# Kernel optimization log

Measured on AMD Instinct MI355X. Metric: run time of the kernel, lower is better.

Reference implementation:

```python
import jax, jax.numpy as jnp
import numpy as np
from jax import lax

B, N, FIN, T, K, FC, FT = 8, 2048, 3, 12, 3, 64, 64


def _conv2d(x, w, b, pad):
    # x [B,C,N,T], w [O,I,1,kw], NCHW conv
    y = lax.conv_general_dilated(x, w, (1, 1), pad,
                                 dimension_numbers=('NCHW', 'OIHW', 'NCHW'))
    return y + b[None, :, None, None]


def _spatial_att(h, W, a, alpha, concat):
    # GAT-style dense attention. h [B,N,Fin], W [Fin,D], a [2D,1]
    D = W.shape[1]
    Wh = h @ W                                             # [B,N,D]
    e = jax.nn.leaky_relu(Wh @ a[:D] + jnp.swapaxes(Wh @ a[D:], 1, 2), alpha)  # [B,N,N]
    att = jax.nn.softmax(jax.nn.sigmoid(e), axis=1)        # softmax over dim=1 (as in torch)
    hp = jnp.einsum('bij,bjd->bid', att, Wh)
    return jax.nn.elu(hp) if concat else hp


def setup_inputs() -> dict:
    key = jax.random.key(0)
    ks = jax.random.split(key, 24)
    rnd = lambda i, shape, scale=1.0: (jax.random.normal(ks[i], shape, dtype=jnp.float32) * scale)
    FTm = FC * T  # 768 spatial-attention feature dim
    D = FTm // 2
    return {
        'x': rnd(0, (B, N, FIN, T)),
        'cheb': rnd(1, (K, N, N), 1.0 / np.sqrt(N)),
        'Gamma': rnd(2, (K, FIN, FC), 1.0 / np.sqrt(FIN)),
        'W_heads': rnd(3, (2, FTm, D), 1.0 / np.sqrt(FTm)),
        'a_heads': rnd(4, (2, 2 * D, 1), 1.0 / np.sqrt(2 * D)),
        'W_out': rnd(5, (FTm, FTm), 1.0 / np.sqrt(FTm)),
        'a_out': rnd(6, (2 * FTm, 1), 1.0 / np.sqrt(2 * FTm)),
        'U1': rnd(7, (FT, FT), 1.0 / np.sqrt(FT)),
        'U2': rnd(8, (FT,), 1.0 / np.sqrt(FT)),
        'U3': rnd(9, (FT,), 1.0 / np.sqrt(FT)),
        'be': rnd(10, (1, T, T), 0.1),
        'Ve': rnd(11, (T, T), 1.0 / np.sqrt(T)),
        'time_w': rnd(12, (FT, FC, 1, 3), 1.0 / np.sqrt(3 * FC)),
        'time_b': rnd(13, (FT,), 0.01),
        'res_w': rnd(14, (FT, FIN, 1, 1), 1.0 / np.sqrt(FIN)),
        'res_b': rnd(15, (FT,), 0.01),
        'back_w': rnd(16, (FT, FC, 1, 3), 1.0 / np.sqrt(3 * FC)),
        'back_b': rnd(17, (FT,), 0.01),
        'fore_w': rnd(18, (FT, FC, 1, 3), 1.0 / np.sqrt(3 * FC)),
        'fore_b': rnd(19, (FT,), 0.01),
        'ln_g': jnp.ones((FT,), jnp.float32),
        'ln_b': jnp.zeros((FT,), jnp.float32),
    }


def reference(x, cheb, Gamma, W_heads, a_heads, W_out, a_out, U1, U2, U3, be, Ve,
              time_w, time_b, res_w, res_b, back_w, back_b, fore_w, fore_b, ln_g, ln_b):
    b, n, fin, t = x.shape
    k_ = cheb.shape[0]
    fc = Gamma.shape[2]
    # ChebNetII interpolation coefficients T_k(x_j), x_j = cos((j+0.5)pi/K) -> [j,k]
    jj = np.arange(k_)
    cxj = jnp.asarray(np.cos(np.outer((jj + 0.5) * np.pi / k_, np.arange(k_))), x.dtype)
    lhs = jnp.einsum('jio,jk->kio', Gamma, cxj)                         # [K,Fin,Fc]
    rhs = jnp.einsum('bnit,knm->kbmit', x, cheb)                        # [K,B,N,Fin,T]
    spatial_gcn = jax.nn.relu((2.0 / (k_ + 1)) * jnp.einsum('kbmit,kio->bmot', rhs, lhs))  # [B,N,Fc,T]

    # Spatial transformer: 2 GAT heads + output attention
    h = spatial_gcn.reshape(b, n, fc * t)
    heads = jax.vmap(lambda W, a: _spatial_att(h, W, a, 0.1, True))(W_heads, a_heads)  # [H,B,N,D]
    hcat = jnp.transpose(heads, (1, 2, 0, 3)).reshape(b, n, -1)
    gcn_SAt = jax.nn.relu(_spatial_att(hcat, W_out, a_out, 0.1, False)).reshape(b, n, fc, t)

    # Temporal conv (1x3, pad 1)
    tc = _conv2d(jnp.transpose(gcn_SAt, (0, 2, 1, 3)), time_w, time_b, ((0, 0), (1, 1)))
    tc = jnp.transpose(tc, (0, 2, 1, 3))                                # [B,N,Ft,T]

    # Temporal attention
    lhs_t = jnp.einsum('bnft,fg,g->btn', tc, U1, U2)                    # [B,T,N]
    rhs_t = jnp.einsum('f,bnft->bnt', U3, tc)                           # [B,N,T]
    prod = jnp.einsum('bsn,bnt->bst', lhs_t, rhs_t)                     # [B,T,T]
    E = jnp.einsum('is,bst->bit', Ve, jax.nn.sigmoid(prod + be))
    E = jax.nn.softmax(E, axis=1)
    tcn = jnp.einsum('bnft,bts->bnfs', tc, E)                           # [B,N,Ft,T]

    # Residual (1x1 conv) + LayerNorm over channel dim
    x_res = _conv2d(jnp.transpose(x, (0, 2, 1, 3)), res_w, res_b, ((0, 0), (0, 0)))
    x_res = jnp.transpose(x_res, (0, 2, 1, 3))                          # [B,N,Ft,T]
    z = jnp.transpose(jax.nn.relu(x_res + tcn), (0, 3, 1, 2))           # [B,T,N,Ft]
    mu = z.mean(-1, keepdims=True)
    var = z.var(-1, keepdims=True)
    z = (z - mu) / jnp.sqrt(var + 1e-5) * ln_g + ln_b
    result = jnp.transpose(z, (0, 2, 3, 1))                             # [B,N,Ft,T]

    rp = jnp.transpose(result, (0, 2, 1, 3))
    backcast = jnp.transpose(_conv2d(rp, back_w, back_b, ((0, 0), (1, 1))), (0, 2, 1, 3))
    forecast = jnp.transpose(_conv2d(rp, fore_w, fore_b, ((0, 0), (1, 1))), (0, 2, 1, 3))
    return (backcast, forecast)
```

## Files before the change

kernel.cpp:

```cpp
#include <hip/hip_runtime.h>


typedef unsigned short u16;
typedef __bf16 bf16x8 __attribute__((ext_vector_type(8)));
typedef float f32x4 __attribute__((ext_vector_type(4)));
typedef u16 u16x8 __attribute__((ext_vector_type(8)));

__device__ __forceinline__ u16 f2b(float f) {
  union { float f; unsigned u; } v; v.f = f;
  unsigned u = v.u;
  u = u + 0x7FFFu + ((u >> 16) & 1u);
  return (u16)(u >> 16);
}
__device__ __forceinline__ float b2f(u16 h) {
  union { unsigned u; float f; } v; v.u = ((unsigned)h) << 16; return v.f;
}
__device__ __forceinline__ float qfun(float x) {
  float e = x > 0.f ? x : 0.1f * x;
  float s = __builtin_amdgcn_rcpf(1.f + __expf(-e));
  return __expf(s);
}

template <int N> __device__ __forceinline__ void waitvm() {
  if constexpr (N == 0)      asm volatile("s_waitcnt vmcnt(0)" ::: "memory");
  else if constexpr (N == 2) asm volatile("s_waitcnt vmcnt(2)" ::: "memory");
  else if constexpr (N == 4) asm volatile("s_waitcnt vmcnt(4)" ::: "memory");
  else if constexpr (N == 6) asm volatile("s_waitcnt vmcnt(6)" ::: "memory");
  else                       asm volatile("s_waitcnt vmcnt(8)" ::: "memory");
}
__device__ __forceinline__ void rawbar() { asm volatile("s_barrier" ::: "memory"); }

#define GLOAD16(g, l) __builtin_amdgcn_global_load_lds( \
    (__attribute__((address_space(1))) void*)(g),       \
    (__attribute__((address_space(3))) void*)(l), 16, 0, 0)

constexpr size_t OFF_LHS     = 0x0;
constexpr size_t OFF_U1U2    = 0x1000;
constexpr size_t OFF_BIASBIG = 0x1100;
constexpr size_t OFF_FH      = 0x3000;
constexpr size_t OFF_GH      = 0x23000;
constexpr size_t OFF_RDH     = 0x43000;
constexpr size_t OFF_FO      = 0x63000;
constexpr size_t OFF_GO      = 0x73000;
constexpr size_t OFF_RDO     = 0x83000;
constexpr size_t OFF_LHST    = 0x93000;
constexpr size_t OFF_RHST    = 0x153000;
constexpr size_t OFF_PROD    = 0x213000;
constexpr size_t OFF_E       = 0x215000;
constexpr size_t OFF_WCATT   = 0x220000;
constexpr size_t OFF_WOUTT   = 0x340000;
constexpr size_t OFF_WTBIG   = 0x460000;
constexpr size_t OFF_XCOLT   = 0x580000;
constexpr size_t OFF_CHEBT   = 0x700000;
constexpr size_t OFF_C1      = 0x1F00000;
constexpr size_t OFF_H       = 0x4300000;
constexpr size_t OFF_P       = 0x700000;
constexpr size_t OFF_WHCATT  = 0x5B00000;
constexpr size_t OFF_HCAT    = 0x7300000;
constexpr size_t OFF_WHOUTT  = 0x5B00000;
constexpr size_t OFF_GCNB    = 0x7300000;
constexpr size_t OFF_WBFBIG  = 0x8B00000;
constexpr size_t OFF_TCS     = 0x700000;
constexpr size_t OFF_RESULTB = 0x3700000;
constexpr size_t WS_NEEDED   = 0x8D40000;

struct GemmP {
  const u16* A; const u16* BT;
  long sA, sB;
  int K, lda, ldb;
  int swz, splitK;
  float* Cf; long sCf; int ldcf;
  u16* Cb;  long sCb; int ldcb;
  u16* CbT; int ldcT; long sCbT;
  const float* bias;
  float* outB; float* outF;
};

template <int EPI, int WN, int AF = 0>
__global__ __launch_bounds__(256, (WN == 1 ? 3 : 2)) void gemm_bf16(GemmP p) {
  constexpr int BUFU  = AF ? (WN == 1 ? 4096 : 8192) : (WN == 1 ? 8192 : 12288);
  constexpr int SMEMU = 3 * BUFU;
  constexpr int LPWB  = AF ? (WN == 1 ? 2 : 4) : (WN == 1 ? 4 : 6);
  constexpr int WVN   = AF ? (LPWB + 4) : LPWB;
  __shared__ u16 smem[SMEMU];
  const int tid  = threadIdx.x;
  const int lane = tid & 63;
  const int wid  = tid >> 6;
  const int wm = wid >> 1, wn = wid & 1;

  long m0, n0;
  int z = blockIdx.z;
  if (p.swz == 2) {
    int nT = gridDim.x;
    int nwg = nT * gridDim.y;
    long L = (long)blockIdx.z * nwg + blockIdx.x + (long)nT * blockIdx.y;
    z = (int)(L & 7);
    long r = L >> 3;
    m0 = (r / nT) * 128;
    n0 = (r % nT) * (128 * WN);
  } else if (p.swz) {
    int nT = gridDim.x;
    int nwg = nT * gridDim.y;
    int lin = blockIdx.x + nT * blockIdx.y;
    int q = nwg >> 3;
    int swz = (lin & 7) * q + (lin >> 3);
    m0 = (long)(swz / nT) * 128;
    n0 = (long)(swz % nT) * (128 * WN);
  } else {
    m0 = (long)blockIdx.y * 128;
    n0 = (long)blockIdx.x * (128 * WN);
  }

  const int K = p.K;
  long aBase, bBase;
  if (p.splitK) {
    int kz = z >> 2, ch = z & 3;
    aBase = (long)kz * p.sA + (long)ch * 512;
    bBase = (long)ch * 512;
  } else {
    aBase = (long)z * p.sA;
    bBase = (long)z * p.sB;
  }
  const u16* Ab = p.A + aBase + m0 * p.lda;
  const u16* Bb = p.BT + bBase + n0 * p.ldb;

  const int sk = (((lane & 3) ^ ((lane >> 3) & 3))) * 8;
  const u16* aP0 = Ab + (long)(wid * 32 + (lane >> 2)) * p.lda + sk;
  const u16* aP1 = aP0 + (long)16 * p.lda;
  const u16* bP0 = Bb + (long)(wid * 32 * WN + (lane >> 2)) * p.ldb + sk;
  const u16* bP1 = bP0 + (long)16 * p.ldb;
  const u16* bP2 = bP0 + (long)32 * p.ldb;
  const u16* bP3 = bP0 + (long)48 * p.ldb;
  const int aslot = wid * 1024;
  const int bslot = (AF ? 0 : 4096) + wid * (WN == 1 ? 1024 : 2048);

  auto STAGE = [&](int s, int bi) {
    long ko = (long)s * 32;
    u16* base = smem + bi * BUFU;
    if constexpr (!AF) {
      GLOAD16(aP0 + ko, base + aslot);
      GLOAD16(aP1 + ko, base + aslot + 512);
    }
    GLOAD16(bP0 + ko, base + bslot);
    GLOAD16(bP1 + ko, base + bslot + 512);
    if constexpr (WN == 2) {
      GLOAD16(bP2 + ko, base + bslot + 1024);
      GLOAD16(bP3 + ko, base + bslot + 1536);
    }
  };

  f32x4 acc[4][4 * WN];
  f32x4 zero = {0.f, 0.f, 0.f, 0.f};
#pragma unroll
  for (int i = 0; i < 4; ++i)
#pragma unroll
    for (int j = 0; j < 4 * WN; ++j) acc[i][j] = zero;

  const int xorc = (lane >> 1) & 3;
  const int aoff = (wm * 64 + (lane & 15)) * 32 + ((lane >> 4) ^ xorc) * 8;
  const int boff = (AF ? 0 : 4096) + (wn * 64 * WN + (lane & 15)) * 32 + ((lane >> 4) ^ xorc) * 8;

  const int nsteps = K >> 5;
  int cur = 0;

  if constexpr (AF) {
    const long kt512 = (long)(K >> 5) * 512;
    const u16* aPf = p.A + (long)z * p.sA + ((m0 >> 4) + wm * 4) * kt512 + lane * 8;
    bf16x8 avA[4], avB[4];
#pragma unroll
    for (int mi = 0; mi < 4; ++mi) avA[mi] = *(const bf16x8*)(aPf + mi * kt512);
    STAGE(0, 0);
#pragma unroll
    for (int mi = 0; mi < 4; ++mi) avB[mi] = *(const bf16x8*)(aPf + mi * kt512 + 512);
    STAGE(1, 1);
    waitvm<WVN>();
    rawbar();

    auto STEPAF = [&](int i, bf16x8 (&av)[4]) {
      const u16* buf = smem + cur * BUFU;
      bf16x8 bv[4 * WN];
#pragma unroll
      for (int ni = 0; ni < 4 * WN; ++ni) bv[ni] = *(const bf16x8*)&buf[boff + ni * 512];
#pragma unroll
      for (int mi = 0; mi < 4; ++mi)
#pragma unroll
        for (int ni = 0; ni < 4 * WN; ++ni)
          acc[mi][ni] = __builtin_amdgcn_mfma_f32_16x16x32_bf16(av[mi], bv[ni], acc[mi][ni], 0, 0, 0);
      if (i + 1 < nsteps) {
        if (i + 2 < nsteps) {
          STAGE(i + 2, cur == 0 ? 2 : cur - 1);
#pragma unroll
          for (int mi = 0; mi < 4; ++mi)
            av[mi] = *(const bf16x8*)(aPf + mi * kt512 + (long)(i + 2) * 512);
          waitvm<WVN>();
        } else {
          waitvm<0>();
        }
        rawbar();
      }
      cur = (cur == 2) ? 0 : cur + 1;
    };
    for (int i = 0; i < nsteps; i += 2) {
      STEPAF(i, avA);
      if (i + 1 < nsteps) STEPAF(i + 1, avB);
    }
  } else {
    STAGE(0, 0);
    STAGE(1, 1);
    waitvm<WVN>();
    rawbar();
    for (int i = 0; i < nsteps; ++i) {
      const u16* buf = smem + cur * BUFU;
      bf16x8 av[4], bv[4 * WN];
#pragma unroll
      for (int mi = 0; mi < 4; ++mi) av[mi] = *(const bf16x8*)&buf[aoff + mi * 512];
#pragma unroll
      for (int ni = 0; ni < 4 * WN; ++ni) bv[ni] = *(const bf16x8*)&buf[boff + ni * 512];
#pragma unroll
      for (int mi = 0; mi < 4; ++mi)
#pragma unroll
        for (int ni = 0; ni < 4 * WN; ++ni)
          acc[mi][ni] = __builtin_amdgcn_mfma_f32_16x16x32_bf16(av[mi], bv[ni], acc[mi][ni], 0, 0, 0);
      if (i + 1 < nsteps) {
        if (i + 2 < nsteps) {
          STAGE(i + 2, cur == 0 ? 2 : cur - 1);
          waitvm<WVN>();
        } else {
          waitvm<0>();
        }
        rawbar();
      }
      cur = (cur == 2) ? 0 : cur + 1;
    }
  }
  __syncthreads();

  if constexpr (EPI == 1) {
#pragma unroll
    for (int h = 0; h < 2; ++h) {
      if (h == 1) __syncthreads();
      if (WN == 1 || wn == h) {
#pragma unroll
        for (int mi = 0; mi < 4; ++mi)
#pragma unroll
          for (int ni = 0; ni < 4 * WN; ++ni) {
            int cl = (WN == 1 ? wn * 64 : 0) + ni * 16 + (lane & 15);
            int mlb = wm * 64 + mi * 16 + ((lane >> 4) << 2);
#pragma unroll
            for (int r = 0; r < 4; ++r)
              smem[cl * 136 + mlb + r] = f2b(acc[mi][ni][r]);
          }
      }
      __syncthreads();
      int c = tid >> 1, half = tid & 1;
      long bat = m0 >> 11;
      u16* dst = p.CbT + bat * p.sCbT + (long)(n0 + h * 128 + c) * p.ldcT +
                 (m0 & 2047) + half * 64;
      const u16* srcp = &smem[c * 136 + half * 64];
#pragma unroll
      for (int j = 0; j < 64; j += 8)
        *(u16x8*)(dst + j) = *(const u16x8*)(srcp + j);
      if (WN == 1) break;
    }
    return;
  }

  if constexpr (EPI == 7) {
    const int q = lane >> 4, g4 = (lane >> 2) & 3, j = lane & 3;
    const int back = ((int)n0 < 768);
    float* obase = (back ? p.outB : p.outF) - (back ? 0 : 768);
#pragma unroll
    for (int mi = 0; mi < 4; ++mi) {
      long rb0 = m0 + wm * 64 + mi * 16 + q * 4;
#pragma unroll
      for (int ni = 0; ni < 4 * WN; ++ni) {
        int cb = (int)n0 + wn * 64 * WN + ni * 16 + g4 * 4;
        f32x4 v = acc[mi][ni];
        float bsv = p.bias[cb + j];
        v[0] += bsv; v[1] += bsv; v[2] += bsv; v[3] += bsv;
#pragma unroll
        for (int d = 1; d <= 2; d <<= 1) {
          f32x4 t;
#pragma unroll
          for (int b = 0; b < 4; ++b) t[b] = __shfl_xor(v[b ^ d], d, 64);
#pragma unroll
          for (int b = 0; b < 4; ++b) if ((lane ^ b) & d) v[b] = t[b];
        }
        *(f32x4*)(obase + (rb0 + j) * 768 + cb) = v;
      }
    }
    return;
  }

#pragma unroll
  for (int mi = 0; mi < 4; ++mi) {
    long rb0 = m0 + wm * 64 + mi * 16 + ((lane >> 4) << 2);
#pragma unroll
    for (int ni = 0; ni < 4 * WN; ++ni) {
      int col = (int)n0 + wn * 64 * WN + ni * 16 + (lane & 15);
#pragma unroll
      for (int r = 0; r < 4; ++r) {
        float v = acc[mi][ni][r];
        long row = rb0 + r;
        if constexpr (EPI == 2) {
          float e = v > 0.f ? v : expm1f(v);
          p.Cb[(long)z * p.sCb + row * p.ldcb + col] = f2b(e);
        } else if constexpr (EPI == 6) {
          p.Cb[row * 768 + col] = f2b(v + p.bias[col & 63]);
        } else if constexpr (EPI == 9) {
          p.Cb[(long)z * p.sCb + row * p.ldcb + col] = f2b(v);
        } else {
          p.Cb[(long)z * p.sCb + row * p.ldcb + col] = f2b(fmaxf(v, 0.f));
        }
      }
    }
  }
}

__global__ void k_prep(const float* Gamma, const float* U1, const float* U2,
                       const float* back_b, const float* fore_b,
                       float* lhs, float* u1u2, float* biasBig) {
  int o = threadIdx.x;
  if (o < 64) {
    const float cx[3][3] = {{1.f, 0.86602540378443871f, 0.5f},
                            {1.f, 6.123233995736766e-17f, -1.f},
                            {1.f, -0.86602540378443871f, 0.5f}};
    for (int k = 0; k < 3; ++k)
      for (int i = 0; i < 3; ++i) {
        float s = 0;
        for (int j = 0; j < 3; ++j) s += Gamma[(j * 3 + i) * 64 + o] * cx[j][k];
        lhs[(k * 3 + i) * 64 + o] = s;
      }
    float s = 0;
    for (int g = 0; g < 64; ++g) s += U1[o * 64 + g] * U2[g];
    u1u2[o] = s;
    for (int t = 0; t < 12; ++t) {
      biasBig[o * 12 + t] = back_b[o];
      biasBig[768 + o * 12 + t] = fore_b[o];
    }
  }
}

__global__ void k_convert(const float* W_heads, const float* W_out, const float* time_w,
                          const float* back_w, const float* fore_w, const float* xg,
                          u16* WcatT, u16* WoutT, u16* WtBig, u16* WbfBig, u16* xcolT) {
  const int N1 = 589824, NT = 589824, NBF = 1179648, N5 = 786432;
  const int TOT = 2 * N1 + NT + NBF + N5;
  for (int o = blockIdx.x * 256 + threadIdx.x; o < TOT; o += gridDim.x * 256) {
    if (o < N1) {
      int dcol = o / 768, kk = o % 768;
      int hd = dcol / 384, d = dcol % 384;
      WcatT[o] = f2b(W_heads[((long)hd * 768 + kk) * 384 + d]);
    } else if (o < 2 * N1) {
      int o2 = o - N1; int dcol = o2 / 768, kk = o2 % 768;
      WoutT[o2] = f2b(W_out[kk * 768 + dcol]);
    } else if (o < 2 * N1 + NT) {
      int o3 = o - 2 * N1; int col = o3 / 768, kk = o3 % 768;
      int t = col >> 6, ft = col & 63, fc = kk / 12, tau = kk % 12;
      int r = tau - t + 1;
      WtBig[o3] = f2b((r >= 0 && r < 3) ? time_w[ft * 192 + fc * 3 + r] : 0.f);
    } else if (o < 2 * N1 + NT + NBF) {
      int o4 = o - 2 * N1 - NT; int col = o4 / 768, kk = o4 % 768;
      int rem = (col < 768) ? col : col - 768;
      int c = rem / 12, tt = rem % 12;
      int fc = kk / 12, tau = kk % 12; int r = tau - tt + 1;
      const float* wsrc = (col < 768) ? back_w : fore_w;
      WbfBig[o4] = f2b((r >= 0 && r < 3) ? wsrc[c * 192 + fc * 3 + r] : 0.f);
    } else {
      int o5 = o - 2 * N1 - NT - NBF; int c = o5 / 2048, n = o5 % 2048;
      float v = 0.f;
      if (c < 288) {
        int b = c / 36, r2 = c % 36, i = r2 / 12, t = r2 % 12;
        v = xg[(long)(b * 2048 + n) * 36 + i * 12 + t];
      }
      xcolT[o5] = f2b(v);
    }
  }
}

__global__ void k_chebT(const float* cheb, u16* chebT) {
  __shared__ float ts[32][33];
  int n0 = blockIdx.x * 32, m0 = blockIdx.y * 32, k = blockIdx.z;
  int c = threadIdx.x & 31, rq = threadIdx.x >> 5;
  const long base = (long)k * 2048 * 2048;
  for (int q = 0; q < 4; ++q) {
    int n = n0 + rq + q * 8;
    ts[rq + q * 8][c] = cheb[base + (long)n * 2048 + m0 + c];
  }
  __syncthreads();
  for (int q = 0; q < 4; ++q) {
    int m = m0 + rq + q * 8;
    chebT[base + (long)m * 2048 + n0 + c] = f2b(ts[c][rq + q * 8]);
  }
}

__global__ __launch_bounds__(256) void k_h(const u16* C1, const float* lhs, u16* h) {
  int bn = blockIdx.x; int b = bn >> 11, n = bn & 2047;
  int tid = threadIdx.x;
  __shared__ float c1s[108], ls[576];
  if (tid < 108) {
    int kk = tid / 12, t = tid % 12; int k = kk / 3, i = kk % 3;
    float s = 0;
#pragma unroll
    for (int ch = 0; ch < 4; ++ch)
      s += b2f(C1[((long)(k * 4 + ch) * 2048 + n) * 384 + b * 36 + i * 12 + t]);
    c1s[tid] = s;
  }
  for (int s = tid; s < 576; s += 256) ls[s] = lhs[s];
  __syncthreads();
  for (int q = 0; q < 3; ++q) {
    int idx = tid + q * 256; int o = idx / 12, t = idx % 12;
    float s = 0;
#pragma unroll
    for (int kk = 0; kk < 9; ++kk) s += c1s[kk * 12 + t] * ls[kk * 64 + o];
    s *= 0.5f;
    if (s < 0.f) s = 0.f;
    h[(long)bn * 768 + idx] = f2b(s);
  }
}

__global__ __launch_bounds__(256) void k_fg(const u16* WhT, int dOff, int Dlen,
                                            const float* aF, const float* aG,
                                            float* fOut, float* gOut) {
  int b = blockIdx.y;
  int i = blockIdx.x * 256 + threadIdx.x;
  __shared__ float af[768], ag[768];
  for (int s = threadIdx.x; s < Dlen; s += 256) { af[s] = aF[s]; ag[s] = aG[s]; }
  __syncthreads();
  const u16* wp = WhT + ((long)b * 768 + dOff) * 2048 + i;
  float fs = 0, gs = 0;
  for (int d = 0; d < Dlen; ++d) {
    float w = b2f(wp[(long)d * 2048]);
    fs += w * af[d]; gs += w * ag[d];
  }
  fOut[b * 2048 + i] = fs;
  gOut[b * 2048 + i] = gs;
}

__global__ __launch_bounds__(256) void k_denom(const float* f, const float* g, float* rd) {
  int b = blockIdx.y;
  int jl = threadIdx.x & 63, ch = threadIdx.x >> 6;
  int j = blockIdx.x * 64 + jl;
  __shared__ float fl[2048];
  __shared__ float red[256];
  for (int s = threadIdx.x; s < 2048; s += 256) fl[s] = f[b * 2048 + s];
  __syncthreads();
  float gj = g[b * 2048 + j];
  float acc = 0;
  for (int i = ch * 512; i < ch * 512 + 512; ++i) acc += qfun(fl[i] + gj);
  red[threadIdx.x] = acc;
  __syncthreads();
  if (ch == 0) {
    float s = red[jl] + red[jl + 64] + red[jl + 128] + red[jl + 192];
    rd[b * 2048 + j] = 1.f / s;
  }
}

__global__ __launch_bounds__(256) void k_Pfrag(const float* f, const float* g,
                                               const float* rd, u16* P) {
  int z = blockIdx.z, mt = blockIdx.y;
  int wid = threadIdx.x >> 6, lane = threadIdx.x & 63;
  int kt = blockIdx.x * 4 + wid;
  const float* fb = f + z * 2048;
  const float* gb = g + z * 2048;
  const float* rb = rd + z * 2048;
  float fv = fb[mt * 16 + (lane & 15)];
  int k0 = kt * 32 + (lane >> 4) * 8;
  float4 g0 = *(const float4*)(gb + k0);
  float4 g1 = *(const float4*)(gb + k0 + 4);
  float4 r0 = *(const float4*)(rb + k0);
  float4 r1 = *(const float4*)(rb + k0 + 4);
  u16x8 o;
  o[0] = f2b(qfun(fv + g0.x) * r0.x);
  o[1] = f2b(qfun(fv + g0.y) * r0.y);
  o[2] = f2b(qfun(fv + g0.z) * r0.z);
  o[3] = f2b(qfun(fv + g0.w) * r0.w);
  o[4] = f2b(qfun(fv + g1.x) * r1.x);
  o[5] = f2b(qfun(fv + g1.y) * r1.y);
  o[6] = f2b(qfun(fv + g1.z) * r1.z);
  o[7] = f2b(qfun(fv + g1.w) * r1.w);
  *(u16x8*)(P + (long)z * 4194304 + ((long)(mt * 64 + kt)) * 512 + lane * 8) = o;
}

__global__ void k_temporal(const u16* tc, const float* u1u2, const float* U3g,
                           float* lhs_t, float* rhs_t) {
  __shared__ float uu[64], u3[64];
  int tid = threadIdx.x;
  if (tid < 64) { uu[tid] = u1u2[tid]; u3[tid] = U3g[tid]; }
  __syncthreads();
  int gid = blockIdx.x * 256 + tid;
  const u16* p = tc + (long)gid * 64;
  float s1 = 0, s2 = 0;
#pragma unroll
  for (int c = 0; c < 8; ++c) {
    u16x8 vv = *(const u16x8*)(p + c * 8);
#pragma unroll
    for (int j = 0; j < 8; ++j) {
      float v = b2f(vv[j]);
      s1 += v * uu[c * 8 + j]; s2 += v * u3[c * 8 + j];
    }
  }
  int t = gid % 12; long bn = gid / 12;
  int b = (int)(bn >> 11);
  lhs_t[((long)b * 12 + t) * 2048 + (int)(bn & 2047)] = s1;
  rhs_t[gid] = s2;
}

__global__ void k_prod(const float* lhs_t, const float* rhs_t, float* prod) {
  int bi = blockIdx.x;
  int b = bi / 144; int r = bi % 144; int s = r / 12; int u = r % 12;
  int tid = threadIdx.x;
  float acc = 0;
  const float* lp = lhs_t + ((long)b * 12 + s) * 2048;
  const float* rp = rhs_t + (long)b * 2048 * 12 + u;
  for (int n = tid; n < 2048; n += 256) acc += lp[n] * rp[n * 12];
  __shared__ float red[256];
  red[tid] = acc; __syncthreads();
  for (int st = 128; st > 0; st >>= 1) {
    if (tid < st) red[tid] += red[tid + st];
    __syncthreads();
  }
  if (tid == 0) prod[bi] = red[0];
}

__global__ void k_E(const float* prod, const float* be, const float* Ve, float* E) {
  int b = blockIdx.x; int tid = threadIdx.x;
  __shared__ float S0[144], E1[144], mx[12], dn[12];
  if (tid < 144) {
    float v = prod[b * 144 + tid] + be[tid];
    S0[tid] = 1.f / (1.f + __expf(-v));
  }
  __syncthreads();
  if (tid < 144) {
    int i = tid / 12, t = tid % 12;
    float a = 0;
    for (int s = 0; s < 12; ++s) a += Ve[i * 12 + s] * S0[s * 12 + t];
    E1[tid] = a;
  }
  __syncthreads();
  if (tid < 12) {
    float m = -1e30f;
    for (int i = 0; i < 12; ++i) m = fmaxf(m, E1[i * 12 + tid]);
    float d = 0;
    for (int i = 0; i < 12; ++i) d += __expf(E1[i * 12 + tid] - m);
    mx[tid] = m; dn[tid] = d;
  }
  __syncthreads();
  if (tid < 144) {
    int t = tid % 12;
    E[b * 144 + tid] = __expf(E1[tid] - mx[t]) / dn[t];
  }
}

__global__ __launch_bounds__(256) void k_res_ln(const u16* tc, const float* E,
                                                const float* xg, const float* res_w,
                                                const float* res_b, const float* ln_g,
                                                const float* ln_b, u16* result) {
  int bn = blockIdx.x; int b = bn >> 11;
  int tid = threadIdx.x;
  __shared__ float tcb[768], Eb[144], xl[36], rw[192], rb[64], lg[64], lb[64], zl[768], mu[12], rs[12];
  for (int s = tid; s < 768; s += 256) tcb[s] = b2f(tc[(long)bn * 768 + s]);
  if (tid < 144) Eb[tid] = E[b * 144 + tid];
  if (tid < 36) xl[tid] = xg[(long)bn * 36 + tid];
  if (tid >= 64 && tid < 256) { int q = tid - 64; if (q < 192) rw[q] = res_w[q]; }
  if (tid < 64) { rb[tid] = res_b[tid]; lg[tid] = ln_g[tid]; lb[tid] = ln_b[tid]; }
  __syncthreads();
  float z[3];
#pragma unroll
  for (int q = 0; q < 3; ++q) {
    int idx = tid + q * 256; int f = idx / 12, s = idx % 12;
    float tcn = 0;
#pragma unroll
    for (int t = 0; t < 12; ++t) tcn += tcb[t * 64 + f] * Eb[t * 12 + s];
    float xr = rb[f];
#pragma unroll
    for (int i = 0; i < 3; ++i) xr += rw[f * 3 + i] * xl[i * 12 + s];
    float v = xr + tcn;
    v = v > 0.f ? v : 0.f;
    z[q] = v; zl[idx] = v;
  }
  __syncthreads();
  if (tid < 12) {
    float m = 0, m2 = 0;
    for (int f = 0; f < 64; ++f) { float v = zl[f * 12 + tid]; m += v; m2 += v * v; }
    m *= (1.f / 64.f); m2 *= (1.f / 64.f);
    mu[tid] = m;
    float var = m2 - m * m;
    rs[tid] = rsqrtf((var > 0.f ? var : 0.f) + 1e-5f);
  }
  __syncthreads();
#pragma unroll
  for (int q = 0; q < 3; ++q) {
    int idx = tid + q * 256; int f = idx / 12, s = idx % 12;
    result[(long)bn * 768 + idx] = f2b((z[q] - mu[s]) * rs[s] * lg[f] + lb[f]);
  }
}

__global__ void k_sentinel(float* out, long n) {
  long i = (long)blockIdx.x * 256 + threadIdx.x;
  if (i < n) out[i] = 12345.0f;
}

extern "C" void kernel_launch(void* const* d_in, const int* in_sizes, int n_in,
                              void* d_out, int out_size, void* d_ws, size_t ws_size,
                              hipStream_t stream) {
  (void)in_sizes; (void)n_in;
  const float* x       = (const float*)d_in[0];
  const float* cheb    = (const float*)d_in[1];
  const float* Gamma   = (const float*)d_in[2];
  const float* W_heads = (const float*)d_in[3];
  const float* a_heads = (const float*)d_in[4];
  const float* W_out   = (const float*)d_in[5];
  const float* a_out   = (const float*)d_in[6];
  const float* U1      = (const float*)d_in[7];
  const float* U2      = (const float*)d_in[8];
  const float* U3      = (const float*)d_in[9];
  const float* be      = (const float*)d_in[10];
  const float* Ve      = (const float*)d_in[11];
  const float* time_w  = (const float*)d_in[12];
  const float* time_b  = (const float*)d_in[13];
  const float* res_w   = (const float*)d_in[14];
  const float* res_b   = (const float*)d_in[15];
  const float* back_w  = (const float*)d_in[16];
  const float* back_b  = (const float*)d_in[17];
  const float* fore_w  = (const float*)d_in[18];
  const float* fore_b  = (const float*)d_in[19];
  const float* ln_g    = (const float*)d_in[20];
  const float* ln_b    = (const float*)d_in[21];
  float* out = (float*)d_out;

  if (ws_size < WS_NEEDED) {
    k_sentinel<<<(out_size + 255) / 256, 256, 0, stream>>>(out, out_size);
    return;
  }

  char* ws = (char*)d_ws;
  float* lhs     = (float*)(ws + OFF_LHS);
  float* u1u2    = (float*)(ws + OFF_U1U2);
  float* biasBig = (float*)(ws + OFF_BIASBIG);
  float* fH      = (float*)(ws + OFF_FH);
  float* gH      = (float*)(ws + OFF_GH);
  float* rdH     = (float*)(ws + OFF_RDH);
  float* fO      = (float*)(ws + OFF_FO);
  float* gO      = (float*)(ws + OFF_GO);
  float* rdO     = (float*)(ws + OFF_RDO);
  float* lhs_t   = (float*)(ws + OFF_LHST);
  float* rhs_t   = (float*)(ws + OFF_RHST);
  float* prod    = (float*)(ws + OFF_PROD);
  float* Ebuf    = (float*)(ws + OFF_E);
  u16* WcatT   = (u16*)(ws + OFF_WCATT);
  u16* WoutT   = (u16*)(ws + OFF_WOUTT);
  u16* WtBig   = (u16*)(ws + OFF_WTBIG);
  u16* WbfBig  = (u16*)(ws + OFF_WBFBIG);
  u16* xcolT   = (u16*)(ws + OFF_XCOLT);
  u16* chebT   = (u16*)(ws + OFF_CHEBT);
  u16* C1      = (u16*)(ws + OFF_C1);
  u16* hbuf    = (u16*)(ws + OFF_H);
  u16* Pbuf    = (u16*)(ws + OFF_P);
  u16* WhcatT  = (u16*)(ws + OFF_WHCATT);
  u16* hcat    = (u16*)(ws + OFF_HCAT);
  u16* WhoutT  = (u16*)(ws + OFF_WHOUTT);
  u16* gcnB    = (u16*)(ws + OFF_GCNB);
  u16* tcsB    = (u16*)(ws + OFF_TCS);
  u16* resultB = (u16*)(ws + OFF_RESULTB);

  k_prep<<<1, 64, 0, stream>>>(Gamma, U1, U2, back_b, fore_b, lhs, u1u2, biasBig);
  k_convert<<<2048, 256, 0, stream>>>(W_heads, W_out, time_w, back_w, fore_w, x,
                                      WcatT, WoutT, WtBig, WbfBig, xcolT);
  k_chebT<<<dim3(64, 64, 3), 256, 0, stream>>>(cheb, chebT);

  {
    GemmP p{}; p.A = chebT; p.BT = xcolT; p.sA = 2048L * 2048; p.sB = 0;
    p.K = 512; p.lda = 2048; p.ldb = 2048; p.splitK = 1; p.swz = 1;
    p.Cb = C1; p.sCb = 2048L * 384; p.ldcb = 384;
    gemm_bf16<9, 1><<<dim3(3, 16, 12), 256, 0, stream>>>(p);
  }
  k_h<<<16384, 256, 0, stream>>>(C1, lhs, hbuf);

  {
    GemmP p{}; p.A = hbuf; p.BT = WcatT; p.sA = 0; p.sB = 0;
    p.K = 768; p.lda = 768; p.ldb = 768; p.swz = 1;
    p.CbT = WhcatT; p.ldcT = 2048; p.sCbT = 768L * 2048;
    gemm_bf16<1, 2><<<dim3(3, 128, 1), 256, 0, stream>>>(p);
  }
  k_fg<<<dim3(8, 8), 256, 0, stream>>>(WhcatT, 0, 384, a_heads, a_heads + 384, fH, gH);
  k_fg<<<dim3(8, 8), 256, 0, stream>>>(WhcatT, 384, 384, a_heads + 768, a_heads + 1152,
                                       fH + 16384, gH + 16384);
  for (int hd = 0; hd < 2; ++hd) {
    const float* f = fH + hd * 16384; const float* g = gH + hd * 16384;
    float* rd = rdH + hd * 16384;
    k_denom<<<dim3(32, 8), 256, 0, stream>>>(f, g, rd);
    k_Pfrag<<<dim3(16, 128, 8), 256, 0, stream>>>(f, g, rd, Pbuf);
    GemmP p{}; p.A = Pbuf; p.BT = WhcatT + (long)hd * 384 * 2048;
    p.sA = 2048L * 2048; p.sB = 768L * 2048;
    p.K = 2048; p.lda = 2048; p.ldb = 2048; p.swz = 2;
    p.Cb = hcat + hd * 384; p.sCb = 2048L * 768; p.ldcb = 768;
    gemm_bf16<2, 1, 1><<<dim3(3, 16, 8), 256, 0, stream>>>(p);
  }

  {
    GemmP p{}; p.A = hcat; p.BT = WoutT; p.sA = 0; p.sB = 0;
    p.K = 768; p.lda = 768; p.ldb = 768; p.swz = 1;
    p.CbT = WhoutT; p.ldcT = 2048; p.sCbT = 768L * 2048;
    gemm_bf16<1, 2><<<dim3(3, 128, 1), 256, 0, stream>>>(p);
  }
  k_fg<<<dim3(8, 8), 256, 0, stream>>>(WhoutT, 0, 768, a_out, a_out + 768, fO, gO);
  k_denom<<<dim3(32, 8), 256, 0, stream>>>(fO, gO, rdO);
  k_Pfrag<<<dim3(16, 128, 8), 256, 0, stream>>>(fO, gO, rdO, Pbuf);
  {
    GemmP p{}; p.A = Pbuf; p.BT = WhoutT; p.sA = 2048L * 2048; p.sB = 768L * 2048;
    p.K = 2048; p.lda = 2048; p.ldb = 2048; p.swz = 2;
    p.Cb = gcnB; p.sCb = 2048L * 768; p.ldcb = 768;
    gemm_bf16<8, 2, 1><<<dim3(3, 16, 8), 256, 0, stream>>>(p);
  }

  {
    GemmP p{}; p.A = gcnB; p.BT = WtBig; p.sA = 0; p.sB = 0;
    p.K = 768; p.lda = 768; p.ldb = 768; p.swz = 1;
    p.Cb = tcsB; p.bias = time_b;
    gemm_bf16<6, 2><<<dim3(3, 128, 1), 256, 0, stream>>>(p);
  }

  k_temporal<<<768, 256, 0, stream>>>(tcsB, u1u2, U3, lhs_t, rhs_t);
  k_prod<<<1152, 256, 0, stream>>>(lhs_t, rhs_t, prod);
  k_E<<<8, 256, 0, stream>>>(prod, be, Ve, Ebuf);

  k_res_ln<<<16384, 256, 0, stream>>>(tcsB, Ebuf, x, res_w, res_b, ln_g, ln_b, resultB);

  {
    GemmP p{}; p.A = resultB; p.BT = WbfBig; p.sA = 0; p.sB = 0;
    p.K = 768; p.lda = 768; p.ldb = 768; p.swz = 1;
    p.bias = biasBig; p.outB = out; p.outF = out + 12582912L;
    gemm_bf16<7, 2><<<dim3(6, 128, 1), 256, 0, stream>>>(p);
  }
}
```

Measured before the change: 702.4 us.

## Write h and LayerNorm outputs in MFMA fragment layout and batch 16 rows per block

k_h and k_res_ln now process 16 rows per block, stage bf16 outputs in shared memory, and write them out pre-swizzled into the fragment-tiled A-operand layout. The two GEMMs that consume them switch to the template variant that reads fragment-ordered A. The aim is to remove the strided A loads and LDS reshuffling in those GEMMs and to cut block launch count. In exchange, k_res_ln serialises 16 rows with several barriers each, which lowers parallelism inside that kernel.

Result: slower. 722.2 us (+2.8%).

```diff
diff --git a/kernel.cpp b/kernel.cpp
--- a/kernel.cpp
+++ b/kernel.cpp
@@ -395,27 +395,42 @@
 }
 
 __global__ __launch_bounds__(256) void k_h(const u16* C1, const float* lhs, u16* h) {
-  int bn = blockIdx.x; int b = bn >> 11, n = bn & 2047;
+  int mf = blockIdx.x;
   int tid = threadIdx.x;
-  __shared__ float c1s[108], ls[576];
-  if (tid < 108) {
-    int kk = tid / 12, t = tid % 12; int k = kk / 3, i = kk % 3;
-    float s = 0;
+  __shared__ float c1s[16][108];
+  __shared__ float ls[576];
+  __shared__ u16 outb[12288];
+  int b = (mf * 16) >> 11;
+  for (int s = tid; s < 1728; s += 256) {
+    int row = s / 108, rr = s % 108;
+    int kk = rr / 12, t = rr % 12; int k = kk / 3, i = kk % 3;
+    int n = (mf * 16 + row) & 2047;
+    float acc = 0;
 #pragma unroll
     for (int ch = 0; ch < 4; ++ch)
-      s += b2f(C1[((long)(k * 4 + ch) * 2048 + n) * 384 + b * 36 + i * 12 + t]);
-    c1s[tid] = s;
+      acc += b2f(C1[((long)(k * 4 + ch) * 2048 + n) * 384 + b * 36 + i * 12 + t]);
+    c1s[row][rr] = acc;
   }
   for (int s = tid; s < 576; s += 256) ls[s] = lhs[s];
   __syncthreads();
-  for (int q = 0; q < 3; ++q) {
-    int idx = tid + q * 256; int o = idx / 12, t = idx % 12;
-    float s = 0;
-#pragma unroll
-    for (int kk = 0; kk < 9; ++kk) s += c1s[kk * 12 + t] * ls[kk * 64 + o];
-    s *= 0.5f;
-    if (s < 0.f) s = 0.f;
-    h[(long)bn * 768 + idx] = f2b(s);
+  for (int row = 0; row < 16; ++row) {
+#pragma unroll
+    for (int j = 0; j < 3; ++j) {
+      int e = j * 256 + tid; int o = e / 12, t = e % 12;
+      float s = 0;
+#pragma unroll
+      for (int kk = 0; kk < 9; ++kk) s += c1s[row][kk * 12 + t] * ls[kk * 64 + o];
+      s *= 0.5f;
+      outb[row * 768 + e] = f2b(s < 0.f ? 0.f : s);
+    }
+  }
+  __syncthreads();
+  for (int q = 0; q < 6; ++q) {
+    int idx = q * 256 + tid;
+    int kt = idx >> 6, lane = idx & 63;
+    int m = lane & 15, koct = lane >> 4;
+    *(u16x8*)(h + ((long)mf * 24 + kt) * 512 + lane * 8) =
+        *(const u16x8*)&outb[m * 768 + kt * 32 + koct * 8];
   }
 }
 
@@ -556,43 +571,57 @@
                                                 const float* xg, const float* res_w,
                                                 const float* res_b, const float* ln_g,
                                                 const float* ln_b, u16* result) {
-  int bn = blockIdx.x; int b = bn >> 11;
-  int tid = threadIdx.x;
-  __shared__ float tcb[768], Eb[144], xl[36], rw[192], rb[64], lg[64], lb[64], zl[768], mu[12], rs[12];
-  for (int s = tid; s < 768; s += 256) tcb[s] = b2f(tc[(long)bn * 768 + s]);
+  int mf = blockIdx.x; int tid = threadIdx.x;
+  int b = (mf * 16) >> 11;
+  __shared__ float Eb[144], rw[192], rb[64], lg[64], lb[64];
+  __shared__ float tcb[768], zl[768], xl[36], mu[12], rs[12];
+  __shared__ u16 outb[12288];
   if (tid < 144) Eb[tid] = E[b * 144 + tid];
-  if (tid < 36) xl[tid] = xg[(long)bn * 36 + tid];
-  if (tid >= 64 && tid < 256) { int q = tid - 64; if (q < 192) rw[q] = res_w[q]; }
+  if (tid < 192) rw[tid] = res_w[tid];
   if (tid < 64) { rb[tid] = res_b[tid]; lg[tid] = ln_g[tid]; lb[tid] = ln_b[tid]; }
-  __syncthreads();
-  float z[3];
-#pragma unroll
-  for (int q = 0; q < 3; ++q) {
-    int idx = tid + q * 256; int f = idx / 12, s = idx % 12;
-    float tcn = 0;
-#pragma unroll
-    for (int t = 0; t < 12; ++t) tcn += tcb[t * 64 + f] * Eb[t * 12 + s];
-    float xr = rb[f];
-#pragma unroll
-    for (int i = 0; i < 3; ++i) xr += rw[f * 3 + i] * xl[i * 12 + s];
-    float v = xr + tcn;
-    v = v > 0.f ? v : 0.f;
-    z[q] = v; zl[idx] = v;
-  }
-  __syncthreads();
-  if (tid < 12) {
-    float m = 0, m2 = 0;
-    for (int f = 0; f < 64; ++f) { float v = zl[f * 12 + tid]; m += v; m2 += v * v; }
-    m *= (1.f / 64.f); m2 *= (1.f / 64.f);
-    mu[tid] = m;
-    float var = m2 - m * m;
-    rs[tid] = rsqrtf((var > 0.f ? var : 0.f) + 1e-5f);
-  }
-  __syncthreads();
-#pragma unroll
-  for (int q = 0; q < 3; ++q) {
-    int idx = tid + q * 256; int f = idx / 12, s = idx % 12;
-    result[(long)bn * 768 + idx] = f2b((z[q] - mu[s]) * rs[s] * lg[f] + lb[f]);
+  for (int r = 0; r < 16; ++r) {
+    long bn = (long)mf * 16 + r;
+    __syncthreads();
+    for (int s = tid; s < 768; s += 256) tcb[s] = b2f(tc[bn * 768 + s]);
+    if (tid < 36) xl[tid] = xg[bn * 36 + tid];
+    __syncthreads();
+    float z[3];
+#pragma unroll
+    for (int q = 0; q < 3; ++q) {
+      int idx = tid + q * 256; int f = idx / 12, s = idx % 12;
+      float tcn = 0;
+#pragma unroll
+      for (int t = 0; t < 12; ++t) tcn += tcb[t * 64 + f] * Eb[t * 12 + s];
+      float xr = rb[f];
+#pragma unroll
+      for (int i = 0; i < 3; ++i) xr += rw[f * 3 + i] * xl[i * 12 + s];
+      float v = xr + tcn;
+      v = v > 0.f ? v : 0.f;
+      z[q] = v; zl[idx] = v;
+    }
+    __syncthreads();
+    if (tid < 12) {
+      float m = 0, m2 = 0;
+      for (int f = 0; f < 64; ++f) { float v = zl[f * 12 + tid]; m += v; m2 += v * v; }
+      m *= (1.f / 64.f); m2 *= (1.f / 64.f);
+      mu[tid] = m;
+      float var = m2 - m * m;
+      rs[tid] = rsqrtf((var > 0.f ? var : 0.f) + 1e-5f);
+    }
+    __syncthreads();
+#pragma unroll
+    for (int q = 0; q < 3; ++q) {
+      int idx = tid + q * 256; int f = idx / 12, s = idx % 12;
+      outb[r * 768 + idx] = f2b((z[q] - mu[s]) * rs[s] * lg[f] + lb[f]);
+    }
+  }
+  __syncthreads();
+  for (int q = 0; q < 6; ++q) {
+    int idx = q * 256 + tid;
+    int kt = idx >> 6, lane = idx & 63;
+    int m = lane & 15, koct = lane >> 4;
+    *(u16x8*)(result + ((long)mf * 24 + kt) * 512 + lane * 8) =
+        *(const u16x8*)&outb[m * 768 + kt * 32 + koct * 8];
   }
 }
 
@@ -675,13 +704,13 @@
     p.Cb = C1; p.sCb = 2048L * 384; p.ldcb = 384;
     gemm_bf16<9, 1><<<dim3(3, 16, 12), 256, 0, stream>>>(p);
   }
-  k_h<<<16384, 256, 0, stream>>>(C1, lhs, hbuf);
+  k_h<<<1024, 256, 0, stream>>>(C1, lhs, hbuf);
 
   {
     GemmP p{}; p.A = hbuf; p.BT = WcatT; p.sA = 0; p.sB = 0;
     p.K = 768; p.lda = 768; p.ldb = 768; p.swz = 1;
     p.CbT = WhcatT; p.ldcT = 2048; p.sCbT = 768L * 2048;
-    gemm_bf16<1, 2><<<dim3(3, 128, 1), 256, 0, stream>>>(p);
+    gemm_bf16<1, 2, 1><<<dim3(3, 128, 1), 256, 0, stream>>>(p);
   }
   k_fg<<<dim3(8, 8), 256, 0, stream>>>(WhcatT, 0, 384, a_heads, a_heads + 384, fH, gH);
   k_fg<<<dim3(8, 8), 256, 0, stream>>>(WhcatT, 384, 384, a_heads + 768, a_heads + 1152,
@@ -725,12 +754,12 @@
   k_prod<<<1152, 256, 0, stream>>>(lhs_t, rhs_t, prod);
   k_E<<<8, 256, 0, stream>>>(prod, be, Ve, Ebuf);
 
-  k_res_ln<<<16384, 256, 0, stream>>>(tcsB, Ebuf, x, res_w, res_b, ln_g, ln_b, resultB);
+  k_res_ln<<<1024, 256, 0, stream>>>(tcsB, Ebuf, x, res_w, res_b, ln_g, ln_b, resultB);
 
   {
     GemmP p{}; p.A = resultB; p.BT = WbfBig; p.sA = 0; p.sB = 0;
     p.K = 768; p.lda = 768; p.ldb = 768; p.swz = 1;
     p.bias = biasBig; p.outB = out; p.outF = out + 12582912L;
-    gemm_bf16<7, 2><<<dim3(6, 128, 1), 256, 0, stream>>>(p);
-  }
-}
+    gemm_bf16<7, 2, 1><<<dim3(6, 128, 1), 256, 0, stream>>>(p);
+  }
+}
```
